# Kernel tuning notes

Hardware: AMD Instinct MI355X
Metric: run time of the kernel (lower is better)

## Reference

```python
import jax, jax.numpy as jnp
import numpy as np

B, C, N = 2, 29, 8192
S, K = 1024, 16  # npoint, nsample
D = C + 3


def fps(xyz_t, npoint):
    # xyz_t: [B, N, 3] -> indices [B, npoint] (furthest point sampling, starts at idx 0)
    b, n, _ = xyz_t.shape

    def step(carry, _):
        dists, farthest = carry  # [B,N], [B]
        centroid = jnp.take_along_axis(xyz_t, farthest[:, None, None], axis=1)  # [B,1,3]
        d = jnp.sum((xyz_t - centroid) ** 2, axis=-1)  # [B,N]
        dists = jnp.minimum(dists, d)
        nxt = jnp.argmax(dists, axis=-1)
        return (dists, nxt), farthest

    init = (jnp.full((b, n), 1e10, xyz_t.dtype), jnp.zeros((b,), jnp.int32))
    _, idx = jax.lax.scan(step, init, None, length=npoint)
    return jnp.transpose(idx)  # [B, npoint]


def knn_self(pts, k):
    # pts: [B, S, 3] -> k nearest neighbor indices within the same set, [B, S, k]
    sq = jnp.sum(pts * pts, axis=-1)
    d2 = sq[:, :, None] + sq[:, None, :] - 2.0 * jnp.einsum('bic,bjc->bij', pts, pts)
    _, idx = jax.lax.top_k(-d2, k)
    return idx


def group(arr, idx):
    # arr: [B, C, N], idx: [B, S, K] -> [B, C, S, K]
    return jax.vmap(lambda a, i: a[:, i])(arr, idx)


def squeeze_2x2(x):
    # RealNVP alt-order squeeze: [n, c, h, w] -> [n, 4c, h/2, w/2]
    tl = x[:, :, 0::2, 0::2]
    br = x[:, :, 1::2, 1::2]
    tr = x[:, :, 0::2, 1::2]
    bl = x[:, :, 1::2, 0::2]
    return jnp.concatenate([tl, br, tr, bl], axis=1)


def conv2d(x, w):
    return jax.lax.conv_general_dilated(
        x, w, window_strides=(1, 1), padding='VALID',
        dimension_numbers=('NCHW', 'OIHW', 'NCHW'))


def setup_inputs() -> dict:
    key = jax.random.key(0)
    ks = jax.random.split(key, 6)
    return {
        'xyz': jax.random.normal(ks[0], (B, 3, N), jnp.float32),
        'feats': jax.random.normal(ks[1], (B, C, N), jnp.float32),
        'w0': jax.random.normal(ks[2], (64, 2 * D * 4, 3, 3), jnp.float32) * 0.02,
        'w1': jax.random.normal(ks[3], (64, 64, 3, 3), jnp.float32) * 0.02,
        'w2': jax.random.normal(ks[4], (128, 64, 3, 3), jnp.float32) * 0.02,
        'w3': jax.random.normal(ks[5], (128, 128, 2, 2), jnp.float32) * 0.02,
    }


def reference(xyz, feats, w0, w1, w2, w3):
    b, c, n = feats.shape
    xyz_t = jnp.transpose(xyz, (0, 2, 1))  # [B,N,3]
    fps_idx = fps(xyz_t, S)  # [B,S]
    new_xyz = jnp.take_along_axis(xyz, fps_idx[:, None, :], axis=2)  # [B,3,S]
    new_xyz_t = jnp.transpose(new_xyz, (0, 2, 1))  # [B,S,3]
    idx = knn_self(new_xyz_t, K)  # [B,S,K], values in [0,S)

    pos_grouped = group(new_xyz, idx)  # [B,3,S,K]
    feats_grouped = group(feats, idx)  # [B,C,S,K] (indices < S, as in original)
    pos_diff = pos_grouped - new_xyz[:, :, :, None]
    fg = jnp.concatenate([pos_diff, feats_grouped], axis=1)  # [B,D,S,K]

    # pairwise outer-product features; second half ([fg;1] x [fg;1] upper block) is all ones
    outer = jnp.einsum('bdsi,bdsj->bdsij', fg, fg)  # [B,D,S,K,K]
    mat = jnp.concatenate([outer, jnp.ones_like(outer)], axis=1)  # [B,2D,S,K,K]
    mat = jnp.transpose(mat, (0, 2, 1, 3, 4)).reshape(b * S, 2 * D, K, K)
    mat = squeeze_2x2(mat)  # [B*S, 8D, K/2, K/2]

    for w in (w0, w1, w2, w3):  # use_bn=False -> Identity bns; spatial 8->6->4->2->1
        mat = jax.nn.relu(conv2d(mat, w))

    new_points = jnp.transpose(mat.reshape(b, S, -1), (0, 2, 1))  # [B,128,S]
    return new_xyz, new_points, fps_idx
```

## Files before the change

kernel.cpp:

```cpp
#include <hip/hip_runtime.h>
#include <hip/hip_bf16.h>

#pragma clang fp contract(off)

#define NPTS 8192
#define NS   1024
#define NB   2
#define NC   29
#define NK   16


__global__ __launch_bounds__(256) void prep_kernel(
    const float* __restrict__ w0, const float* __restrict__ w1,
    const float* __restrict__ w2, const float* __restrict__ w3,
    float* __restrict__ w0t, float* __restrict__ w1t,
    float* __restrict__ w2t, float* __restrict__ w3t,
    float* __restrict__ bias0)
{
    int i = blockIdx.x * 256 + threadIdx.x;
    int n = gridDim.x * 256;
    for (int e = i; e < 73728; e += n) {
        int o = e & 63, r = e >> 6, tap = r % 9, ic2 = r / 9;
        int ic = ((ic2 >> 5) << 6) + (ic2 & 31);
        w0t[e] = w0[(o * 256 + ic) * 9 + tap];
    }
    for (int e = i; e < 36864; e += n) {
        int o = e & 63, r = e >> 6, tap = r % 9, ic = r / 9;
        w1t[e] = w1[(o * 64 + ic) * 9 + tap];
    }
    for (int e = i; e < 73728; e += n) {
        int o = e & 127, r = e >> 7, tap = r % 9, ic = r / 9;
        w2t[e] = w2[(o * 64 + ic) * 9 + tap];
    }
    for (int e = i; e < 65536; e += n) {
        int o = e & 127, r = e >> 7, tap = r & 3, ic = r >> 2;
        w3t[e] = w3[(o * 128 + ic) * 4 + tap];
    }
    if (i < 64) {
        float sum = 0.0f;
        for (int q = 0; q < 4; ++q)
            for (int c = 0; c < 32; ++c)
                for (int t = 0; t < 9; ++t)
                    sum += w0[(i * 256 + q * 64 + 32 + c) * 9 + t];
        bias0[i] = sum;
    }
}

__device__ __forceinline__ float wave_max_nonneg(float x) {
    int v = __float_as_int(x);
    int t;
    t = __builtin_amdgcn_update_dpp(0, v, 0x111, 0xf, 0xf, true);
    v = __float_as_int(fmaxf(__int_as_float(v), __int_as_float(t)));
    t = __builtin_amdgcn_update_dpp(0, v, 0x112, 0xf, 0xf, true);
    v = __float_as_int(fmaxf(__int_as_float(v), __int_as_float(t)));
    t = __builtin_amdgcn_update_dpp(0, v, 0x114, 0xf, 0xf, true);
    v = __float_as_int(fmaxf(__int_as_float(v), __int_as_float(t)));
    t = __builtin_amdgcn_update_dpp(0, v, 0x118, 0xf, 0xf, true);
    v = __float_as_int(fmaxf(__int_as_float(v), __int_as_float(t)));
    t = __builtin_amdgcn_update_dpp(0, v, 0x142, 0xa, 0xf, true);
    v = __float_as_int(fmaxf(__int_as_float(v), __int_as_float(t)));
    t = __builtin_amdgcn_update_dpp(0, v, 0x143, 0xc, 0xf, true);
    v = __float_as_int(fmaxf(__int_as_float(v), __int_as_float(t)));
    return __int_as_float(__builtin_amdgcn_readlane(v, 63));
}

typedef float v2f __attribute__((ext_vector_type(2)));

__global__ __launch_bounds__(256, 1) void fps_kernel(
    const float* __restrict__ xyz,
    float* __restrict__ nx_ws, float* __restrict__ out)
{
    int b = blockIdx.x;
    int tid = threadIdx.x;
    int lane = tid & 63;
    const float* X = xyz + b * 3 * NPTS;

    __shared__ unsigned long long s_key[NS];

    v2f px[16], py[16], pz[16], dist[16];

    for (int i = tid; i < NS; i += 256) s_key[i] = 0ull;
    if (tid == 0) s_key[0] = 0xFFFFFFFFull;

#pragma unroll
    for (int i = 0; i < 16; ++i) {
        int g2 = i * 512 + tid * 2;
        px[i] = *(const v2f*)(X + g2);
        py[i] = *(const v2f*)(X + NPTS + g2);
        pz[i] = *(const v2f*)(X + 2 * NPTS + g2);
        dist[i] = (v2f){1e10f, 1e10f};
    }
    __syncthreads();

    float cx = X[0], cy = X[NPTS], cz = X[2 * NPTS];

    for (int it = 1; it < NS; ++it) {
        v2f c2x = {cx, cx}, c2y = {cy, cy}, c2z = {cz, cz};
#pragma unroll
        for (int i = 0; i < 16; ++i) {
            v2f dx = px[i] - c2x, dy = py[i] - c2y, dz = pz[i] - c2z;
            v2f d = (dx * dx + dy * dy) + dz * dz;
            v2f dd = dist[i];
            dd.x = fminf(dd.x, d.x);
            dd.y = fminf(dd.y, d.y);
            dist[i] = dd;
        }
        float t16[16];
#pragma unroll
        for (int i = 0; i < 16; ++i) t16[i] = fmaxf(dist[i].x, dist[i].y);
        float t8[8];
#pragma unroll
        for (int i = 0; i < 8; ++i) t8[i] = fmaxf(t16[2 * i], t16[2 * i + 1]);
        float t4[4];
#pragma unroll
        for (int i = 0; i < 4; ++i) t4[i] = fmaxf(t8[2 * i], t8[2 * i + 1]);
        float bv = fmaxf(fmaxf(t4[0], t4[1]), fmaxf(t4[2], t4[3]));
        float wm = wave_max_nonneg(bv);
        if (bv == wm) {
            int gi = 0;
#pragma unroll
            for (int i = 15; i >= 0; --i) {
                if (dist[i].y == wm) gi = i * 512 + tid * 2 + 1;
                if (dist[i].x == wm) gi = i * 512 + tid * 2;
            }
            unsigned long long key =
                ((unsigned long long)__float_as_uint(wm) << 32) | (unsigned)(~gi);
            atomicMax(&s_key[it], key);
        }
        __syncthreads();
        int idx = (int)(~(unsigned)s_key[it]);
        cx = X[idx]; cy = X[NPTS + idx]; cz = X[2 * NPTS + idx];
    }

    float* out_fps = out + 268288 + b * NS;
    for (int i = tid; i < NS; i += 256) {
        int j = (int)(~(unsigned)s_key[i]);
        out_fps[i] = (float)j;
        float x = X[j], y = X[NPTS + j], z = X[2 * NPTS + j];
        nx_ws[(b * 3 + 0) * NS + i] = x; out[(b * 3 + 0) * NS + i] = x;
        nx_ws[(b * 3 + 1) * NS + i] = y; out[(b * 3 + 1) * NS + i] = y;
        nx_ws[(b * 3 + 2) * NS + i] = z; out[(b * 3 + 2) * NS + i] = z;
    }
}

__global__ __launch_bounds__(256) void knn_kernel(
    const float* __restrict__ nx_ws, int* __restrict__ knn_ws)
{
    int q = blockIdx.x * 4 + (threadIdx.x >> 6);
    int lane = threadIdx.x & 63;
    int b = q >> 10, s = q & 1023;
    const float* P = nx_ws + b * 3 * NS;
    float qx = P[s], qy = P[NS + s], qz = P[2 * NS + s];
    float sqq = (qx * qx + qy * qy) + qz * qz;
    int base_j = lane * 16;
    float d2[16];
    {
        const float4* x4 = (const float4*)(P + base_j);
        const float4* y4 = (const float4*)(P + NS + base_j);
        const float4* z4 = (const float4*)(P + 2 * NS + base_j);
#pragma unroll
        for (int t = 0; t < 4; ++t) {
            float4 xv = x4[t], yv = y4[t], zv = z4[t];
            float xs[4] = { xv.x, xv.y, xv.z, xv.w };
            float ys[4] = { yv.x, yv.y, yv.z, yv.w };
            float zs[4] = { zv.x, zv.y, zv.z, zv.w };
#pragma unroll
            for (int e = 0; e < 4; ++e) {
                float xj = xs[e], yj = ys[e], zj = zs[e];
                float sqj = (xj * xj + yj * yj) + zj * zj;
                float dot = (qx * xj + qy * yj) + qz * zj;
                d2[t * 4 + e] = (sqq + sqj) - 2.0f * dot;
            }
        }
    }
    for (int r = 0; r < NK; ++r) {
        float lv = 3.0e38f; int li = 0;
#pragma unroll
        for (int i = 0; i < 16; ++i) { if (d2[i] < lv) { lv = d2[i]; li = i; } }
        int gj = base_j + li;
#pragma unroll
        for (int off = 32; off > 0; off >>= 1) {
            float ov = __shfl_xor(lv, off, 64);
            int   oj = __shfl_xor(gj, off, 64);
            if (ov < lv || (ov == lv && oj < gj)) { lv = ov; gj = oj; }
        }
        if (lane == 0) knn_ws[q * NK + r] = gj;
        if ((gj >> 4) == lane) {
            int li2 = gj & 15;
#pragma unroll
            for (int i = 0; i < 16; ++i) if (i == li2) d2[i] = 3.0e38f;
        }
    }
}

template<int GODD>
__device__ __forceinline__ void conv0_accum(
    const float* __restrict__ x0r, const float* __restrict__ wbase, float acc[9])
{
    for (int ic2 = 0; ic2 < 128; ++ic2) {
        const float4* x4 = (const float4*)(x0r + ic2 * 64);
        float rr[32];
#pragma unroll
        for (int j = 0; j < 4; ++j) {
            float4 t0 = x4[j * 2], t1 = x4[j * 2 + 1];
            rr[j*8+0]=t0.x; rr[j*8+1]=t0.y; rr[j*8+2]=t0.z; rr[j*8+3]=t0.w;
            rr[j*8+4]=t1.x; rr[j*8+5]=t1.y; rr[j*8+6]=t1.z; rr[j*8+7]=t1.w;
        }
        float w[9];
#pragma unroll
        for (int t = 0; t < 9; ++t) w[t] = wbase[(ic2 * 9 + t) * 64];
#pragma unroll
        for (int pp = 0; pp < 9; ++pp) {
            const int ly = GODD ? (pp < 3 ? 0 : 1) : (pp < 6 ? 0 : 1);
            const int xx = GODD ? (pp < 3 ? pp + 3 : pp - 3) : (pp < 6 ? pp : pp - 6);
#pragma unroll
            for (int ky = 0; ky < 3; ++ky)
#pragma unroll
                for (int kx = 0; kx < 3; ++kx)
                    acc[pp] = __builtin_fmaf(w[ky * 3 + kx], rr[(ly + ky) * 8 + xx + kx], acc[pp]);
        }
    }
}

__global__ __launch_bounds__(256) void conv_kernel(
    const float* __restrict__ feats, const float* __restrict__ nx_ws,
    const int* __restrict__ knn_ws,
    const float* __restrict__ w0t, const float* __restrict__ bias0,
    const float* __restrict__ w1t, const float* __restrict__ w2t,
    const float* __restrict__ w3t, float* __restrict__ out)
{
    __shared__ float s_fg[512];
    __shared__ int   s_ni[16];
    __shared__ float s_x0[8192];
    __shared__ float s_a1[64 * 36];
    __shared__ float s_a2[64 * 16];
    __shared__ float s_a3[128 * 4];

    int bs = blockIdx.x, b = bs >> 10, s = bs & 1023;
    int tid = threadIdx.x;
    if (tid < 16) s_ni[tid] = knn_ws[bs * NK + tid];
    __syncthreads();
    const float* P = nx_ws + b * 3 * NS;
#pragma unroll
    for (int e = tid; e < 512; e += 256) {
        int d = e >> 4, k = e & 15; int j = s_ni[k];
        float v = (d < 3) ? (P[d * NS + j] - P[d * NS + s])
                          : feats[(b * NC + (d - 3)) * NPTS + j];
        s_fg[e] = v;
    }
    __syncthreads();
    for (int e = tid; e < 8192; e += 256) {
        int ic2 = e >> 6, pos = e & 63, u = pos >> 3, v = pos & 7;
        int q = ic2 >> 5, ch = ic2 & 31;
        int ro = q & 1, co = ((q + 1) >> 1) & 1;
        s_x0[e] = s_fg[ch * 16 + 2 * u + ro] * s_fg[ch * 16 + 2 * v + co];
    }
    __syncthreads();

    int o = tid & 63, g = tid >> 6;
    {
        int r0 = g + (g >> 1);
        float acc[9];
        float bz = bias0[o];
#pragma unroll
        for (int p = 0; p < 9; ++p) acc[p] = bz;
        const float* x0r = s_x0 + r0 * 8;
        const float* wb = w0t + o;
        if (g & 1) conv0_accum<1>(x0r, wb, acc);
        else       conv0_accum<0>(x0r, wb, acc);
#pragma unroll
        for (int pp = 0; pp < 9; ++pp) s_a1[o * 36 + g * 9 + pp] = fmaxf(acc[pp], 0.0f);
    }
    __syncthreads();
    {
        float a[4] = {0, 0, 0, 0};
        const float* wb = w1t + o;
        for (int ic = 0; ic < 64; ++ic) {
            const float2* ar2 = (const float2*)(s_a1 + ic * 36 + g * 6);
            float r[18];
#pragma unroll
            for (int t = 0; t < 9; ++t) { float2 tv = ar2[t]; r[t*2] = tv.x; r[t*2+1] = tv.y; }
            float w[9];
#pragma unroll
            for (int t = 0; t < 9; ++t) w[t] = wb[(ic * 9 + t) * 64];
#pragma unroll
            for (int x = 0; x < 4; ++x)
#pragma unroll
                for (int ky = 0; ky < 3; ++ky)
#pragma unroll
                    for (int kx = 0; kx < 3; ++kx)
                        a[x] = __builtin_fmaf(w[ky * 3 + kx], r[ky * 6 + x + kx], a[x]);
        }
#pragma unroll
        for (int x = 0; x < 4; ++x) s_a2[o * 16 + g * 4 + x] = fmaxf(a[x], 0.0f);
    }
    __syncthreads();
    {
        int o2 = tid & 127, g2 = tid >> 7;
        float a[2] = {0, 0};
        const float* wb = w2t + o2;
        for (int ic = 0; ic < 64; ++ic) {
            const float4* ar4 = (const float4*)(s_a2 + ic * 16 + g2 * 4);
            float r[12];
#pragma unroll
            for (int t = 0; t < 3; ++t) { float4 tv = ar4[t]; r[t*4]=tv.x; r[t*4+1]=tv.y; r[t*4+2]=tv.z; r[t*4+3]=tv.w; }
            float w[9];
#pragma unroll
            for (int t = 0; t < 9; ++t) w[t] = wb[(ic * 9 + t) * 128];
#pragma unroll
            for (int x = 0; x < 2; ++x)
#pragma unroll
                for (int ky = 0; ky < 3; ++ky)
#pragma unroll
                    for (int kx = 0; kx < 3; ++kx)
                        a[x] = __builtin_fmaf(w[ky * 3 + kx], r[ky * 4 + x + kx], a[x]);
        }
#pragma unroll
        for (int x = 0; x < 2; ++x) s_a3[o2 * 4 + g2 * 2 + x] = fmaxf(a[x], 0.0f);
    }
    __syncthreads();
    if (tid < 128) {
        float acc = 0.0f;
        const float* wb = w3t + tid;
        for (int ic = 0; ic < 128; ++ic) {
            float4 av = *(const float4*)(s_a3 + ic * 4);
            float wa = wb[(ic * 4 + 0) * 128];
            float wbv = wb[(ic * 4 + 1) * 128];
            float wc = wb[(ic * 4 + 2) * 128];
            float wd = wb[(ic * 4 + 3) * 128];
            acc = __builtin_fmaf(wa, av.x, acc);
            acc = __builtin_fmaf(wbv, av.y, acc);
            acc = __builtin_fmaf(wc, av.z, acc);
            acc = __builtin_fmaf(wd, av.w, acc);
        }
        out[6144 + (b * 128 + tid) * NS + s] = fmaxf(acc, 0.0f);
    }
}

extern "C" void kernel_launch(void* const* d_in, const int* in_sizes, int n_in,
                              void* d_out, int out_size, void* d_ws, size_t ws_size,
                              hipStream_t stream) {
    const float* xyz   = (const float*)d_in[0];
    const float* feats = (const float*)d_in[1];
    const float* w0    = (const float*)d_in[2];
    const float* w1    = (const float*)d_in[3];
    const float* w2    = (const float*)d_in[4];
    const float* w3    = (const float*)d_in[5];
    float* out = (float*)d_out;

    char* ws = (char*)d_ws;
    float* nx_ws  = (float*)(ws + 8192);
    int*   knn_ws = (int*)(ws + 32768);
    float* w0t    = (float*)(ws + 163840);
    float* bias0  = (float*)(ws + 458752);
    float* w1t    = (float*)(ws + 459008);
    float* w2t    = (float*)(ws + 606464);
    float* w3t    = (float*)(ws + 901376);

    prep_kernel<<<128, 256, 0, stream>>>(w0, w1, w2, w3, w0t, w1t, w2t, w3t, bias0);
    fps_kernel<<<NB, 256, 0, stream>>>(xyz, nx_ws, out);
    knn_kernel<<<(NB * NS) / 4, 256, 0, stream>>>(nx_ws, knn_ws);
    conv_kernel<<<NB * NS, 256, 0, stream>>>(feats, nx_ws, knn_ws, w0t, bias0, w1t, w2t, w3t, out);
}
```

Baseline: 1.720 ms.

## Widen FPS block to 512 threads and cache point cloud in LDS

```diff
diff --git a/kernel.cpp b/kernel.cpp
--- a/kernel.cpp
+++ b/kernel.cpp
@@ -64,53 +64,45 @@
     return __int_as_float(__builtin_amdgcn_readlane(v, 63));
 }
 
-typedef float v2f __attribute__((ext_vector_type(2)));
-
-__global__ __launch_bounds__(256, 1) void fps_kernel(
+__global__ __launch_bounds__(512, 2) void fps_kernel(
     const float* __restrict__ xyz,
     float* __restrict__ nx_ws, float* __restrict__ out)
 {
     int b = blockIdx.x;
     int tid = threadIdx.x;
-    int lane = tid & 63;
     const float* X = xyz + b * 3 * NPTS;
 
+    __shared__ float s_xyz[3 * NPTS];
     __shared__ unsigned long long s_key[NS];
 
-    v2f px[16], py[16], pz[16], dist[16];
-
-    for (int i = tid; i < NS; i += 256) s_key[i] = 0ull;
+    float px[16], py[16], pz[16], dist[16];
+#pragma unroll
+    for (int i = 0; i < 16; ++i) {
+        int gi = i * 512 + tid;
+        float x = X[gi], y = X[NPTS + gi], z = X[2 * NPTS + gi];
+        px[i] = x; py[i] = y; pz[i] = z;
+        dist[i] = 1e10f;
+        s_xyz[gi] = x; s_xyz[NPTS + gi] = y; s_xyz[2 * NPTS + gi] = z;
+    }
+    for (int i = tid; i < NS; i += 512) s_key[i] = 0ull;
     if (tid == 0) s_key[0] = 0xFFFFFFFFull;
-
-#pragma unroll
-    for (int i = 0; i < 16; ++i) {
-        int g2 = i * 512 + tid * 2;
-        px[i] = *(const v2f*)(X + g2);
-        py[i] = *(const v2f*)(X + NPTS + g2);
-        pz[i] = *(const v2f*)(X + 2 * NPTS + g2);
-        dist[i] = (v2f){1e10f, 1e10f};
-    }
-    __syncthreads();
-
-    float cx = X[0], cy = X[NPTS], cz = X[2 * NPTS];
+    __syncthreads();
+
+    float cx = s_xyz[0], cy = s_xyz[NPTS], cz = s_xyz[2 * NPTS];
 
     for (int it = 1; it < NS; ++it) {
-        v2f c2x = {cx, cx}, c2y = {cy, cy}, c2z = {cz, cz};
+#pragma unroll
+        for (int i = 0; i < 16; ++i)
+            asm volatile("" : "+v"(px[i]), "+v"(py[i]), "+v"(pz[i]));
 #pragma unroll
         for (int i = 0; i < 16; ++i) {
-            v2f dx = px[i] - c2x, dy = py[i] - c2y, dz = pz[i] - c2z;
-            v2f d = (dx * dx + dy * dy) + dz * dz;
-            v2f dd = dist[i];
-            dd.x = fminf(dd.x, d.x);
-            dd.y = fminf(dd.y, d.y);
-            dist[i] = dd;
-        }
-        float t16[16];
-#pragma unroll
-        for (int i = 0; i < 16; ++i) t16[i] = fmaxf(dist[i].x, dist[i].y);
+            float dx = px[i] - cx, dy = py[i] - cy, dz = pz[i] - cz;
+            float d = (dx * dx + dy * dy) + dz * dz;
+            dist[i] = fminf(dist[i], d);
+        }
         float t8[8];
 #pragma unroll
-        for (int i = 0; i < 8; ++i) t8[i] = fmaxf(t16[2 * i], t16[2 * i + 1]);
+        for (int i = 0; i < 8; ++i) t8[i] = fmaxf(dist[2 * i], dist[2 * i + 1]);
         float t4[4];
 #pragma unroll
         for (int i = 0; i < 4; ++i) t4[i] = fmaxf(t8[2 * i], t8[2 * i + 1]);
@@ -119,24 +111,22 @@
         if (bv == wm) {
             int gi = 0;
 #pragma unroll
-            for (int i = 15; i >= 0; --i) {
-                if (dist[i].y == wm) gi = i * 512 + tid * 2 + 1;
-                if (dist[i].x == wm) gi = i * 512 + tid * 2;
-            }
+            for (int i = 15; i >= 0; --i)
+                if (dist[i] == wm) gi = i * 512 + tid;
             unsigned long long key =
                 ((unsigned long long)__float_as_uint(wm) << 32) | (unsigned)(~gi);
             atomicMax(&s_key[it], key);
         }
         __syncthreads();
         int idx = (int)(~(unsigned)s_key[it]);
-        cx = X[idx]; cy = X[NPTS + idx]; cz = X[2 * NPTS + idx];
+        cx = s_xyz[idx]; cy = s_xyz[NPTS + idx]; cz = s_xyz[2 * NPTS + idx];
     }
 
     float* out_fps = out + 268288 + b * NS;
-    for (int i = tid; i < NS; i += 256) {
+    for (int i = tid; i < NS; i += 512) {
         int j = (int)(~(unsigned)s_key[i]);
         out_fps[i] = (float)j;
-        float x = X[j], y = X[NPTS + j], z = X[2 * NPTS + j];
+        float x = s_xyz[j], y = s_xyz[NPTS + j], z = s_xyz[2 * NPTS + j];
         nx_ws[(b * 3 + 0) * NS + i] = x; out[(b * 3 + 0) * NS + i] = x;
         nx_ws[(b * 3 + 1) * NS + i] = y; out[(b * 3 + 1) * NS + i] = y;
         nx_ws[(b * 3 + 2) * NS + i] = z; out[(b * 3 + 2) * NS + i] = z;
@@ -358,7 +348,7 @@
     float* w3t    = (float*)(ws + 901376);
 
     prep_kernel<<<128, 256, 0, stream>>>(w0, w1, w2, w3, w0t, w1t, w2t, w3t, bias0);
-    fps_kernel<<<NB, 256, 0, stream>>>(xyz, nx_ws, out);
+    fps_kernel<<<NB, 512, 0, stream>>>(xyz, nx_ws, out);
     knn_kernel<<<(NB * NS) / 4, 256, 0, stream>>>(nx_ws, knn_ws);
     conv_kernel<<<NB * NS, 256, 0, stream>>>(feats, nx_ws, knn_ws, w0t, bias0, w1t, w2t, w3t, out);
 }
```

New measurement: 1.402 ms. -18.5%, faster.
